# Optimization experiments

Hardware: AMD Instinct MI355X
Metric: run time of the kernel (lower is better)

The kernel has to match this reference:

```python
import jax, jax.numpy as jnp
import numpy as np

N_NODES = 100000
N_EDGES = 1600000
D_IN = 128
D_OUT = 128


def setup_inputs() -> dict:
    key = jax.random.key(0)
    k1, k2, k3, k4, k5, k6 = jax.random.split(key, 6)
    stdv = 1.0 / np.sqrt(D_OUT)
    x = jax.random.normal(k1, (N_NODES, D_IN), dtype=jnp.float32)
    weight = jax.random.uniform(k2, (D_IN, D_OUT), minval=-stdv, maxval=stdv, dtype=jnp.float32)
    bias = jax.random.uniform(k3, (D_OUT,), minval=-stdv, maxval=stdv, dtype=jnp.float32)
    edge_vals = jax.random.uniform(k4, (N_EDGES,), dtype=jnp.float32)
    edge_rows = jax.random.randint(k5, (N_EDGES,), 0, N_NODES, dtype=jnp.int32)
    edge_cols = jax.random.randint(k6, (N_EDGES,), 0, N_NODES, dtype=jnp.int32)
    return {"x": x, "weight": weight, "bias": bias,
            "edge_vals": edge_vals, "edge_rows": edge_rows, "edge_cols": edge_cols}


def reference(x, weight, bias, edge_vals, edge_rows, edge_cols):
    # Dense projection: support = X W  -> [N, D_OUT]
    support = jnp.matmul(x, weight)
    # Sparse adjacency matmul (COO SpMM): out[r] += A[r,c] * support[c]
    gathered = edge_vals[:, None] * support[edge_cols]  # [E, D_OUT]
    out = jax.ops.segment_sum(gathered, edge_rows, num_segments=N_NODES)
    return out + bias
```

## Files before the change

kernel.cpp:

```cpp
#include <hip/hip_runtime.h>
#include <hip/hip_bf16.h>

#define N_NODES 100000
#define N_EDGES 1600000
#define D 128
#define NBUCK 782
#define G 320
#define EPB 5000
#define CAPG 16
#define WSLOT (G * CAPG)
#define EBCAP 2816
#define OCAP 8192

typedef short  s8v  __attribute__((ext_vector_type(8)));
typedef float  f4v  __attribute__((ext_vector_type(4)));

__device__ __forceinline__ ushort f2bf(float f) {
    uint u = __float_as_uint(f);
    return (ushort)((u + 0x7FFFu + ((u >> 16) & 1u)) >> 16);
}
__device__ __forceinline__ float bflo(uint u) { return __uint_as_float(u << 16); }
__device__ __forceinline__ float bfhi(uint u) { return __uint_as_float(u & 0xFFFF0000u); }

__global__ __launch_bounds__(256) void k_wt(const float* __restrict__ w,
                                            ushort* __restrict__ wt,
                                            int* __restrict__ ocur) {
    int i = blockIdx.x * 256 + threadIdx.x;
    if (i == 0) *ocur = 0;
    if (i < D * D) {
        int k = i >> 7, n = i & 127;
        wt[n * D + k] = f2bf(w[i]);
    }
}

__global__ __launch_bounds__(256, 4) void k_fuse(const float* __restrict__ x,
                                                 const ushort* __restrict__ wt,
                                                 ushort* __restrict__ supb,
                                                 const int* __restrict__ er,
                                                 const int* __restrict__ ec,
                                                 const float* __restrict__ ev,
                                                 int2* __restrict__ tmp,
                                                 int* __restrict__ counts,
                                                 int* __restrict__ ocur,
                                                 int4* __restrict__ ovf) {
    __shared__ __attribute__((aligned(16))) char smem[32768];

    const int t = (int)threadIdx.x;

    if (blockIdx.x < NBUCK) {
        char* Bl = smem;
        const int lane = t & 63;
        const int w    = t >> 6;
        const int row0 = blockIdx.x * 128;

        const int4* g4 = (const int4*)wt;
        #pragma unroll
        for (int i = 0; i < 8; ++i) {
            int idx = t + i * 256;
            int n = idx >> 4, c = idx & 15;
            *(int4*)(Bl + ((n * 256 + c * 16) ^ ((n & 7) << 4))) = g4[idx];
        }
        __syncthreads();

        f4v acc[2][8] = {};
        const int arow = row0 + w * 32 + (lane & 15);
        const int kb   = (lane >> 4) * 8;

        #pragma unroll
        for (int ks = 0; ks < 4; ++ks) {
            s8v a[2];
            #pragma unroll
            for (int m = 0; m < 2; ++m) {
                int r = arow + m * 16;
                float4 f0 = make_float4(0.f, 0.f, 0.f, 0.f);
                float4 f1 = make_float4(0.f, 0.f, 0.f, 0.f);
                if (r < N_NODES) {
                    const float4* p = (const float4*)(x + (size_t)r * D + ks * 32 + kb);
                    f0 = p[0];
                    f1 = p[1];
                }
                s8v av;
                av[0] = (short)f2bf(f0.x); av[1] = (short)f2bf(f0.y);
                av[2] = (short)f2bf(f0.z); av[3] = (short)f2bf(f0.w);
                av[4] = (short)f2bf(f1.x); av[5] = (short)f2bf(f1.y);
                av[6] = (short)f2bf(f1.z); av[7] = (short)f2bf(f1.w);
                a[m] = av;
            }
            #pragma unroll
            for (int n = 0; n < 8; ++n) {
                int brow = n * 16 + (lane & 15);
                s8v b = *(s8v*)(Bl + ((brow * 256 + (ks * 32 + kb) * 2) ^ ((brow & 7) << 4)));
                acc[0][n] = __builtin_amdgcn_mfma_f32_16x16x32_bf16(a[0], b, acc[0][n], 0, 0, 0);
                acc[1][n] = __builtin_amdgcn_mfma_f32_16x16x32_bf16(a[1], b, acc[1][n], 0, 0, 0);
            }
        }

        __syncthreads();
        char* E = Bl + w * 8192;
        #pragma unroll
        for (int m = 0; m < 2; ++m)
            #pragma unroll
            for (int n = 0; n < 8; ++n)
                #pragma unroll
                for (int r = 0; r < 4; ++r) {
                    int rl  = m * 16 + ((lane >> 4) << 2) + r;
                    int col = n * 16 + (lane & 15);
                    *(ushort*)(E + ((rl * 256 + col * 2) ^ ((rl & 7) << 4))) =
                        f2bf(acc[m][n][r]);
                }
        __syncthreads();
        #pragma unroll
        for (int i = 0; i < 8; ++i) {
            int idx = lane + i * 64;
            int rl = idx >> 4, c = idx & 15;
            int4 v = *(int4*)(E + ((rl * 256 + c * 16) ^ ((rl & 7) << 4)));
            int grow = row0 + w * 32 + rl;
            if (grow < N_NODES)
                *(int4*)((char*)supb + (size_t)grow * 256 + c * 16) = v;
        }
    } else {
        int* cur = (int*)smem;
        const int g = blockIdx.x - NBUCK;
        for (int i = t; i < NBUCK; i += 256) cur[i] = 0;
        __syncthreads();

        const int base = g * EPB;
        for (int i = t; i < EPB; i += 256) {
            int e = base + i;
            int   r = er[e];
            int   c = ec[e];
            float v = ev[e];
            int b = r >> 7;
            int p = atomicAdd(&cur[b], 1);
            if (p < CAPG) {
                tmp[(size_t)b * WSLOT + g * CAPG + p] =
                    make_int2(((r & 127) << 17) | c, __float_as_int(v));
            } else {
                int o = atomicAdd(ocur, 1);
                if (o < OCAP) ovf[o] = make_int4(r, c, __float_as_int(v), 0);
            }
        }
        __syncthreads();
        for (int i = t; i < NBUCK; i += 256) {
            int n = cur[i];
            counts[g * NBUCK + i] = (n > CAPG) ? CAPG : n;
        }
    }
}

__global__ __launch_bounds__(320) void k_sort(int2* __restrict__ tmp,
                                              const int* __restrict__ counts,
                                              int2* __restrict__ rowrg,
                                              int* __restrict__ ocur,
                                              int4* __restrict__ ovf) {
    __shared__ int wn[G];
    __shared__ int wincl[G];
    __shared__ int hist[128], ex[128], cur[128];
    __shared__ int2 eb[EBCAP];
    const int tx = (int)threadIdx.x;
    const int b  = blockIdx.x;
    const int r0 = b << 7;

    int n = counts[tx * NBUCK + b];
    wn[tx] = n;
    wincl[tx] = n;
    if (tx < 128) { hist[tx] = 0; cur[tx] = 0; }
    __syncthreads();

    for (int off = 1; off < G; off <<= 1) {
        int t = (tx >= off) ? wincl[tx - off] : 0;
        __syncthreads();
        wincl[tx] += t;
        __syncthreads();
    }
    const int cnt0 = wincl[G - 1];

    {
        int o = wincl[tx] - wn[tx];
        const int2* win = tmp + ((size_t)b * G + tx) * CAPG;
        for (int k = 0; k < wn[tx]; ++k) {
            int idx = o + k;
            int2 t = win[k];
            if (idx < EBCAP) {
                eb[idx] = t;
            } else {
                int oo = atomicAdd(ocur, 1);
                if (oo < OCAP)
                    ovf[oo] = make_int4(r0 + (t.x >> 17), t.x & 0x1FFFF, t.y, 0);
            }
        }
    }
    __syncthreads();
    const int cnt = (cnt0 > EBCAP) ? EBCAP : cnt0;

    for (int i = tx; i < cnt; i += 320)
        atomicAdd(&hist[eb[i].x >> 17], 1);
    __syncthreads();

    int hv = (tx < 128) ? hist[tx] : 0;
    if (tx < 128) ex[tx] = hv;
    __syncthreads();
    for (int off = 1; off < 128; off <<= 1) {
        int t = 0;
        if (tx < 128 && tx >= off) t = ex[tx - off];
        __syncthreads();
        if (tx < 128) ex[tx] += t;
        __syncthreads();
    }
    if (tx < 128) {
        int incl = ex[tx];
        int e0   = incl - hv;
        if (r0 + tx < N_NODES)
            rowrg[r0 + tx] = make_int2(b * WSLOT + e0, b * WSLOT + incl);
        ex[tx] = e0;
    }
    __syncthreads();

    int2* dst = tmp + (size_t)b * WSLOT;
    for (int i = tx; i < cnt; i += 320) {
        int2 t = eb[i];
        int lr = t.x >> 17;
        int p  = ex[lr] + atomicAdd(&cur[lr], 1);
        dst[p] = make_int2(t.x & 0x1FFFF, t.y);
    }
}

__global__ __launch_bounds__(256) void k_spmm(const ushort* __restrict__ supb,
                                              const int2* __restrict__ rowrg,
                                              const int2* __restrict__ scv,
                                              const float* __restrict__ bias,
                                              float* __restrict__ out) {
    const int row = blockIdx.x * 4 + (threadIdx.x >> 6);
    if (row >= N_NODES) return;
    const int lane = threadIdx.x & 63;
    const int sub  = lane >> 5;
    const int sl   = lane & 31;

    const int2 rg = rowrg[row];
    int j = rg.x;
    const int end = rg.y;
    const uint2* S = (const uint2*)supb;

    float4 acc = make_float4(0.f, 0.f, 0.f, 0.f);

    for (; j + 7 < end; j += 8) {
        int2 e0 = scv[j + sub];
        int2 e1 = scv[j + 2 + sub];
        int2 e2 = scv[j + 4 + sub];
        int2 e3 = scv[j + 6 + sub];
        uint2 s0 = S[(size_t)e0.x * 32 + sl];
        uint2 s1 = S[(size_t)e1.x * 32 + sl];
        uint2 s2 = S[(size_t)e2.x * 32 + sl];
        uint2 s3 = S[(size_t)e3.x * 32 + sl];
        float v0 = __int_as_float(e0.y), v1 = __int_as_float(e1.y);
        float v2 = __int_as_float(e2.y), v3 = __int_as_float(e3.y);
        acc.x += v0 * bflo(s0.x) + v1 * bflo(s1.x) + v2 * bflo(s2.x) + v3 * bflo(s3.x);
        acc.y += v0 * bfhi(s0.x) + v1 * bfhi(s1.x) + v2 * bfhi(s2.x) + v3 * bfhi(s3.x);
        acc.z += v0 * bflo(s0.y) + v1 * bflo(s1.y) + v2 * bflo(s2.y) + v3 * bflo(s3.y);
        acc.w += v0 * bfhi(s0.y) + v1 * bfhi(s1.y) + v2 * bfhi(s2.y) + v3 * bfhi(s3.y);
    }
    for (; j < end; j += 2) {
        int jj = j + sub;
        if (jj > end - 1) jj = end - 1;
        int2 e = scv[jj];
        float v = (j + sub < end) ? __int_as_float(e.y) : 0.f;
        uint2 s = S[(size_t)e.x * 32 + sl];
        acc.x += v * bflo(s.x);
        acc.y += v * bfhi(s.x);
        acc.z += v * bflo(s.y);
        acc.w += v * bfhi(s.y);
    }

    acc.x += __shfl_xor(acc.x, 32);
    acc.y += __shfl_xor(acc.y, 32);
    acc.z += __shfl_xor(acc.z, 32);
    acc.w += __shfl_xor(acc.w, 32);

    if (sub == 0) {
        float4 bb = *(const float4*)(bias + 4 * sl);
        acc.x += bb.x; acc.y += bb.y; acc.z += bb.z; acc.w += bb.w;
        *(float4*)(out + (size_t)row * D + 4 * sl) = acc;
    }
}

__global__ __launch_bounds__(256) void k_ofl(const ushort* __restrict__ supb,
                                             const int4* __restrict__ ovf,
                                             const int* __restrict__ ocur,
                                             float* __restrict__ out) {
    int n = *ocur;
    if (n > OCAP) n = OCAP;
    const int lane = threadIdx.x & 63;
    const uint* S = (const uint*)supb;
    for (int e = (blockIdx.x * 256 + threadIdx.x) >> 6; e < n; e += 64) {
        int4 rec = ovf[e];
        uint s = S[(size_t)rec.y * 64 + lane];
        float v = __int_as_float(rec.z);
        atomicAdd(&out[(size_t)rec.x * D + 2 * lane],     v * bflo(s));
        atomicAdd(&out[(size_t)rec.x * D + 2 * lane + 1], v * bfhi(s));
    }
}

extern "C" void kernel_launch(void* const* d_in, const int* in_sizes, int n_in,
                              void* d_out, int out_size, void* d_ws, size_t ws_size,
                              hipStream_t stream) {
    const float* x    = (const float*)d_in[0];
    const float* w    = (const float*)d_in[1];
    const float* bias = (const float*)d_in[2];
    const float* ev   = (const float*)d_in[3];
    const int*   er   = (const int*)d_in[4];
    const int*   ec   = (const int*)d_in[5];
    float* out = (float*)d_out;

    char* ws = (char*)d_ws;
    ushort* supb   = (ushort*)(ws);
    ushort* wt     = (ushort*)(ws + 25600000);
    int*    counts = (int*)   (ws + 25632768);
    int*    ocur   = (int*)   (ws + 26633728);
    int4*   ovf    = (int4*)  (ws + 26633792);
    int2*   tmp    = (int2*)  (ws + 26764864);
    int2*   rowrg  = (int2*)  (ws + 58795584);

    k_wt  <<<64, 256, 0, stream>>>(w, wt, ocur);
    k_fuse<<<NBUCK + G, 256, 0, stream>>>(x, wt, supb, er, ec, ev, tmp,
                                          counts, ocur, ovf);
    k_sort<<<NBUCK, 320, 0, stream>>>(tmp, counts, rowrg, ocur, ovf);

    k_spmm<<<(N_NODES + 3) / 4, 256, 0, stream>>>(supb, rowrg, tmp, bias, out);
    k_ofl <<<16, 256, 0, stream>>>(supb, ovf, ocur, out);
}
```

Measured before the change: 135.8 us.

## Fuse per-bucket row sort and SpMM into one kernel using LDS edge list

Merges the bucket counting-sort kernel and the row-wise SpMM kernel into one kernel per 128-row bucket. Edges are sorted by local row directly into shared memory and consumed from there, so the sorted list is never written back to global memory and the row-range array and one launch go away. It also drops the prefix scan over producer windows by scanning the fixed-size window slots directly. In exchange there are only 782 blocks of 512 threads, each processing 16 rows per wave serially, which may lower parallelism and latency hiding for the gather. A smaller LDS capacity also pushes more edges to the atomic overflow path.

```diff
diff --git a/kernel.cpp b/kernel.cpp
--- a/kernel.cpp
+++ b/kernel.cpp
@@ -9,7 +9,7 @@
 #define EPB 5000
 #define CAPG 16
 #define WSLOT (G * CAPG)
-#define EBCAP 2816
+#define EBC 2240
 #define OCAP 8192
 
 typedef short  s8v  __attribute__((ext_vector_type(8)));
@@ -148,138 +148,119 @@
     }
 }
 
-__global__ __launch_bounds__(320) void k_sort(int2* __restrict__ tmp,
-                                              const int* __restrict__ counts,
-                                              int2* __restrict__ rowrg,
-                                              int* __restrict__ ocur,
-                                              int4* __restrict__ ovf) {
+__global__ __launch_bounds__(512) void k_ss(const ushort* __restrict__ supb,
+                                            const int2* __restrict__ tmp,
+                                            const int* __restrict__ counts,
+                                            const float* __restrict__ bias,
+                                            float* __restrict__ out,
+                                            int* __restrict__ ocur,
+                                            int4* __restrict__ ovf) {
     __shared__ int wn[G];
-    __shared__ int wincl[G];
     __shared__ int hist[128], ex[128], cur[128];
-    __shared__ int2 eb[EBCAP];
+    __shared__ int2 es[EBC];
     const int tx = (int)threadIdx.x;
     const int b  = blockIdx.x;
     const int r0 = b << 7;
 
-    int n = counts[tx * NBUCK + b];
-    wn[tx] = n;
-    wincl[tx] = n;
+    for (int i = tx; i < G; i += 512) wn[i] = counts[i * NBUCK + b];
     if (tx < 128) { hist[tx] = 0; cur[tx] = 0; }
     __syncthreads();
 
-    for (int off = 1; off < G; off <<= 1) {
-        int t = (tx >= off) ? wincl[tx - off] : 0;
-        __syncthreads();
-        wincl[tx] += t;
-        __syncthreads();
-    }
-    const int cnt0 = wincl[G - 1];
-
-    {
-        int o = wincl[tx] - wn[tx];
-        const int2* win = tmp + ((size_t)b * G + tx) * CAPG;
-        for (int k = 0; k < wn[tx]; ++k) {
-            int idx = o + k;
-            int2 t = win[k];
-            if (idx < EBCAP) {
-                eb[idx] = t;
+    const int2* win = tmp + (size_t)b * WSLOT;
+
+    for (int i = tx; i < WSLOT; i += 512) {
+        if ((i & (CAPG - 1)) < wn[i >> 4])
+            atomicAdd(&hist[win[i].x >> 17], 1);
+    }
+    __syncthreads();
+
+    int hv = (tx < 128) ? hist[tx] : 0;
+    if (tx < 128) ex[tx] = hv;
+    __syncthreads();
+    for (int off = 1; off < 128; off <<= 1) {
+        int t = 0;
+        if (tx < 128 && tx >= off) t = ex[tx - off];
+        __syncthreads();
+        if (tx < 128) ex[tx] += t;
+        __syncthreads();
+    }
+    if (tx < 128) ex[tx] -= hv;
+    __syncthreads();
+
+    for (int i = tx; i < WSLOT; i += 512) {
+        if ((i & (CAPG - 1)) < wn[i >> 4]) {
+            int2 t = win[i];
+            int lr = t.x >> 17;
+            int p  = ex[lr] + atomicAdd(&cur[lr], 1);
+            if (p < EBC) {
+                es[p] = make_int2(t.x & 0x1FFFF, t.y);
             } else {
                 int oo = atomicAdd(ocur, 1);
                 if (oo < OCAP)
-                    ovf[oo] = make_int4(r0 + (t.x >> 17), t.x & 0x1FFFF, t.y, 0);
+                    ovf[oo] = make_int4(r0 + lr, t.x & 0x1FFFF, t.y, 0);
             }
         }
     }
     __syncthreads();
-    const int cnt = (cnt0 > EBCAP) ? EBCAP : cnt0;
-
-    for (int i = tx; i < cnt; i += 320)
-        atomicAdd(&hist[eb[i].x >> 17], 1);
-    __syncthreads();
-
-    int hv = (tx < 128) ? hist[tx] : 0;
-    if (tx < 128) ex[tx] = hv;
-    __syncthreads();
-    for (int off = 1; off < 128; off <<= 1) {
-        int t = 0;
-        if (tx < 128 && tx >= off) t = ex[tx - off];
-        __syncthreads();
-        if (tx < 128) ex[tx] += t;
-        __syncthreads();
-    }
-    if (tx < 128) {
-        int incl = ex[tx];
-        int e0   = incl - hv;
-        if (r0 + tx < N_NODES)
-            rowrg[r0 + tx] = make_int2(b * WSLOT + e0, b * WSLOT + incl);
-        ex[tx] = e0;
-    }
-    __syncthreads();
-
-    int2* dst = tmp + (size_t)b * WSLOT;
-    for (int i = tx; i < cnt; i += 320) {
-        int2 t = eb[i];
-        int lr = t.x >> 17;
-        int p  = ex[lr] + atomicAdd(&cur[lr], 1);
-        dst[p] = make_int2(t.x & 0x1FFFF, t.y);
-    }
-}
-
-__global__ __launch_bounds__(256) void k_spmm(const ushort* __restrict__ supb,
-                                              const int2* __restrict__ rowrg,
-                                              const int2* __restrict__ scv,
-                                              const float* __restrict__ bias,
-                                              float* __restrict__ out) {
-    const int row = blockIdx.x * 4 + (threadIdx.x >> 6);
-    if (row >= N_NODES) return;
-    const int lane = threadIdx.x & 63;
+
+    const int w    = tx >> 6;
+    const int lane = tx & 63;
     const int sub  = lane >> 5;
     const int sl   = lane & 31;
-
-    const int2 rg = rowrg[row];
-    int j = rg.x;
-    const int end = rg.y;
     const uint2* S = (const uint2*)supb;
 
-    float4 acc = make_float4(0.f, 0.f, 0.f, 0.f);
-
-    for (; j + 7 < end; j += 8) {
-        int2 e0 = scv[j + sub];
-        int2 e1 = scv[j + 2 + sub];
-        int2 e2 = scv[j + 4 + sub];
-        int2 e3 = scv[j + 6 + sub];
-        uint2 s0 = S[(size_t)e0.x * 32 + sl];
-        uint2 s1 = S[(size_t)e1.x * 32 + sl];
-        uint2 s2 = S[(size_t)e2.x * 32 + sl];
-        uint2 s3 = S[(size_t)e3.x * 32 + sl];
-        float v0 = __int_as_float(e0.y), v1 = __int_as_float(e1.y);
-        float v2 = __int_as_float(e2.y), v3 = __int_as_float(e3.y);
-        acc.x += v0 * bflo(s0.x) + v1 * bflo(s1.x) + v2 * bflo(s2.x) + v3 * bflo(s3.x);
-        acc.y += v0 * bfhi(s0.x) + v1 * bfhi(s1.x) + v2 * bfhi(s2.x) + v3 * bfhi(s3.x);
-        acc.z += v0 * bflo(s0.y) + v1 * bflo(s1.y) + v2 * bflo(s2.y) + v3 * bflo(s3.y);
-        acc.w += v0 * bfhi(s0.y) + v1 * bfhi(s1.y) + v2 * bfhi(s2.y) + v3 * bfhi(s3.y);
-    }
-    for (; j < end; j += 2) {
-        int jj = j + sub;
-        if (jj > end - 1) jj = end - 1;
-        int2 e = scv[jj];
-        float v = (j + sub < end) ? __int_as_float(e.y) : 0.f;
-        uint2 s = S[(size_t)e.x * 32 + sl];
-        acc.x += v * bflo(s.x);
-        acc.y += v * bfhi(s.x);
-        acc.z += v * bflo(s.y);
-        acc.w += v * bfhi(s.y);
-    }
-
-    acc.x += __shfl_xor(acc.x, 32);
-    acc.y += __shfl_xor(acc.y, 32);
-    acc.z += __shfl_xor(acc.z, 32);
-    acc.w += __shfl_xor(acc.w, 32);
-
-    if (sub == 0) {
-        float4 bb = *(const float4*)(bias + 4 * sl);
-        acc.x += bb.x; acc.y += bb.y; acc.z += bb.z; acc.w += bb.w;
-        *(float4*)(out + (size_t)row * D + 4 * sl) = acc;
+    float4 bb = make_float4(0.f, 0.f, 0.f, 0.f);
+    if (sub == 0) bb = *(const float4*)(bias + 4 * sl);
+
+    for (int rr = 0; rr < 16; ++rr) {
+        const int lr = w * 16 + rr;
+        const int gr = r0 + lr;
+        if (gr >= N_NODES) break;
+
+        int j = ex[lr];
+        int end = j + hist[lr];
+        if (end > EBC) end = EBC;
+
+        float4 acc = make_float4(0.f, 0.f, 0.f, 0.f);
+
+        for (; j + 7 < end; j += 8) {
+            int2 e0 = es[j + sub];
+            int2 e1 = es[j + 2 + sub];
+            int2 e2 = es[j + 4 + sub];
+            int2 e3 = es[j + 6 + sub];
+            uint2 s0 = S[(size_t)e0.x * 32 + sl];
+            uint2 s1 = S[(size_t)e1.x * 32 + sl];
+            uint2 s2 = S[(size_t)e2.x * 32 + sl];
+            uint2 s3 = S[(size_t)e3.x * 32 + sl];
+            float v0 = __int_as_float(e0.y), v1 = __int_as_float(e1.y);
+            float v2 = __int_as_float(e2.y), v3 = __int_as_float(e3.y);
+            acc.x += v0 * bflo(s0.x) + v1 * bflo(s1.x) + v2 * bflo(s2.x) + v3 * bflo(s3.x);
+            acc.y += v0 * bfhi(s0.x) + v1 * bfhi(s1.x) + v2 * bfhi(s2.x) + v3 * bfhi(s3.x);
+            acc.z += v0 * bflo(s0.y) + v1 * bflo(s1.y) + v2 * bflo(s2.y) + v3 * bflo(s3.y);
+            acc.w += v0 * bfhi(s0.y) + v1 * bfhi(s1.y) + v2 * bfhi(s2.y) + v3 * bfhi(s3.y);
+        }
+        for (; j < end; j += 2) {
+            int jj = j + sub;
+            if (jj > end - 1) jj = end - 1;
+            int2 e = es[jj];
+            float v = (j + sub < end) ? __int_as_float(e.y) : 0.f;
+            uint2 s = S[(size_t)e.x * 32 + sl];
+            acc.x += v * bflo(s.x);
+            acc.y += v * bfhi(s.x);
+            acc.z += v * bflo(s.y);
+            acc.w += v * bfhi(s.y);
+        }
+
+        acc.x += __shfl_xor(acc.x, 32);
+        acc.y += __shfl_xor(acc.y, 32);
+        acc.z += __shfl_xor(acc.z, 32);
+        acc.w += __shfl_xor(acc.w, 32);
+
+        if (sub == 0) {
+            float4 o = make_float4(acc.x + bb.x, acc.y + bb.y,
+                                   acc.z + bb.z, acc.w + bb.w);
+            *(float4*)(out + (size_t)gr * D + 4 * sl) = o;
+        }
     }
 }
 
@@ -318,13 +299,10 @@
     int*    ocur   = (int*)   (ws + 26633728);
     int4*   ovf    = (int4*)  (ws + 26633792);
     int2*   tmp    = (int2*)  (ws + 26764864);
-    int2*   rowrg  = (int2*)  (ws + 58795584);
 
     k_wt  <<<64, 256, 0, stream>>>(w, wt, ocur);
     k_fuse<<<NBUCK + G, 256, 0, stream>>>(x, wt, supb, er, ec, ev, tmp,
                                           counts, ocur, ovf);
-    k_sort<<<NBUCK, 320, 0, stream>>>(tmp, counts, rowrg, ocur, ovf);
-
-    k_spmm<<<(N_NODES + 3) / 4, 256, 0, stream>>>(supb, rowrg, tmp, bias, out);
+    k_ss  <<<NBUCK, 512, 0, stream>>>(supb, tmp, counts, bias, out, ocur, ovf);
     k_ofl <<<16, 256, 0, stream>>>(supb, ovf, ocur, out);
 }
```

Result: faster. 121.3 us (-10.7%).
